# Kernel optimization log

Measured on AMD Instinct MI355X. Metric: run time of the kernel, lower is better.

The kernel has to match this reference:

```python
import jax, jax.numpy as jnp
import numpy as np


def setup_inputs() -> dict:
    key = jax.random.key(0)
    ks = jax.random.split(key, 8)
    B, N, D, E, M = 32, 128, 128, 32, 8192
    h_nodes = jax.random.normal(ks[0], (B, N, D), dtype=jnp.float32)
    h_edges = jax.random.normal(ks[1], (B, N, N, E), dtype=jnp.float32)
    W_edit = jax.random.normal(ks[2], (2 * D + E, 4), dtype=jnp.float32) * 0.02
    b_edit = jnp.zeros((4,), dtype=jnp.float32)
    W_stop = jax.random.normal(ks[3], (D, 1), dtype=jnp.float32) * 0.02
    b_stop = jnp.zeros((1,), dtype=jnp.float32)
    i_idx = jax.random.randint(ks[4], (M,), 0, N, dtype=jnp.int32)
    j_idx = jax.random.randint(ks[5], (M,), 0, N, dtype=jnp.int32)
    b_idx = jax.random.randint(ks[6], (M,), 0, 4, dtype=jnp.int32)
    feas = jax.random.randint(ks[7], (B, M), 0, 2, dtype=jnp.int32).astype(jnp.bool_)
    stop_feas = jnp.ones((B,), dtype=jnp.bool_)
    return {
        "h_nodes": h_nodes, "h_edges": h_edges,
        "W_edit": W_edit, "b_edit": b_edit,
        "W_stop": W_stop, "b_stop": b_stop,
        "i_idx": i_idx, "j_idx": j_idx, "b_idx": b_idx,
        "feas": feas, "stop_feas": stop_feas,
    }


def reference(h_nodes, h_edges, W_edit, b_edit, W_stop, b_stop,
              i_idx, j_idx, b_idx, feas, stop_feas):
    # h_nodes: [B,N,D], h_edges: [B,N,N,E]
    B = h_nodes.shape[0]
    M = i_idx.shape[0]
    neg_inf = jnp.asarray(-jnp.inf, dtype=h_nodes.dtype)
    # Batched gather of all (i, j, e_ij) edit features: [B, M, 2D+E]
    feat = jnp.concatenate(
        [h_nodes[:, i_idx], h_nodes[:, j_idx], h_edges[:, i_idx, j_idx]],
        axis=-1,
    )
    # Single fused small matmul over all edits: [B, M, 4]
    edit_logits = jnp.einsum("bmf,fo->bmo", feat, W_edit) + b_edit
    # Select the bond-type channel b for each edit: [B, M]
    sel = jnp.take_along_axis(
        edit_logits, jnp.broadcast_to(b_idx[None, :, None], (B, M, 1)), axis=2
    )[..., 0]
    sel = jnp.where(feas, sel, neg_inf)
    # STOP logit from mean-pooled node features: [B]
    stop = (h_nodes.mean(axis=1) @ W_stop + b_stop)[:, 0]
    stop = jnp.where(stop_feas, stop, neg_inf)
    # [B, M+1] logits (edits followed by STOP)
    return jnp.concatenate([sel, stop[:, None]], axis=1)
```

## Files before the change

### kernel.cpp

```cpp
#include <hip/hip_runtime.h>
#include <hip/hip_fp16.h>
#include <math.h>

#define BATCH 32
#define NNODE 128
#define DDIM 128
#define EDIM 32
#define MEDITS 8192
#define OUTSTRIDE (MEDITS + 1)

typedef unsigned short u16;
typedef unsigned int u32;

#define MASK16 ((u16)0xFBFFu)
#define MASK32 0xC76A6000u

__device__ __forceinline__ u32 f2u(float f) { u32 x; __builtin_memcpy(&x, &f, 4); return x; }
__device__ __forceinline__ float u2f(u32 x) { float f; __builtin_memcpy(&f, &x, 4); return f; }

template <int MODE>
__device__ __forceinline__ float cv16(u32 bits) {
    if constexpr (MODE == 1) return __half2float(__ushort_as_half((u16)bits));
    else                     return u2f(bits << 16);
}
template <int MODE>
__device__ __forceinline__ float cv16hi(u32 w) {
    if constexpr (MODE == 1) return __half2float(__ushort_as_half((u16)(w >> 16)));
    else                     return u2f(w & 0xFFFF0000u);
}

__device__ __forceinline__ u16 f32_to_f16_safe(float f) {
    u16 h = __half_as_ushort(__float2half_rn(f));
    if ((h & 0x7C00u) == 0x7C00u) h = (u16)((h & 0x8000u) | 0x7BFFu);
    return h;
}

__device__ __forceinline__ u16 f32_to_bf16_safe(float f) {
    u32 x = f2u(f);
    u32 r = x + 0x7FFFu + ((x >> 16) & 1u);
    u16 u = (u16)(r >> 16);
    if ((u & 0x7C00u) == 0x7C00u) u = (u16)((u & 0x8000u) | 0x7BFFu);
    return u;
}

__device__ __forceinline__ u32 enc_f32(float f) {
    u32 x = f2u(f);
    if ((x & 0x7F800000u) == 0x7F800000u)
        x = (x & 0x80000000u) | 0x476A6000u;
    return x;
}

template <int MODE>
__device__ __forceinline__ float LD(const void* p, size_t i) {
    if constexpr (MODE == 0) return ((const float*)p)[i];
    else return cv16<MODE>(((const u16*)p)[i]);
}

template <int MODE>
__device__ __forceinline__ void ST(void* o, size_t i, float v, bool masked) {
    if constexpr (MODE == 0) ((u32*)o)[i] = masked ? MASK32 : enc_f32(v);
    else if constexpr (MODE == 1) ((u16*)o)[i] = masked ? MASK16 : f32_to_f16_safe(v);
    else ((u16*)o)[i] = masked ? MASK16 : f32_to_bf16_safe(v);
}

template <int NT>
__device__ __forceinline__ int block_probe(const u16* __restrict__ h) {
    const int t = threadIdx.x;
    __shared__ int cb[4], cs[4];
    int myb = 0, mys = 0;
#pragma unroll
    for (int k = 0; k < 256 / NT; ++k) {
        u16 u = h[2 * (t + k * NT)];
        int e8 = (u >> 7) & 0xFF;
        int e5 = (u >> 10) & 0x1F;
        myb += (e8 >= 118 && e8 <= 129);
        mys += (e5 >= 6 && e5 <= 14);
    }
#pragma unroll
    for (int off = 32; off; off >>= 1) {
        myb += __shfl_down(myb, off, 64);
        mys += __shfl_down(mys, off, 64);
    }
    if ((t & 63) == 0) { cb[t >> 6] = myb; cs[t >> 6] = mys; }
    if (NT < 256 && t == 0) {
#pragma unroll
        for (int w = NT / 64; w < 4; ++w) { cb[w] = 0; cs[w] = 0; }
    }
    __syncthreads();
    int B = cb[0] + cb[1] + cb[2] + cb[3];
    int S = cs[0] + cs[1] + cs[2] + cs[3];
    return (B < 48) ? 0 : ((S > 87) ? 1 : 2);
}

template <int MODE>
__device__ void proj_impl(const void* h_nodes, const void* W_edit, const void* b_edit,
                          const void* W_stop, const void* b_stop,
                          const unsigned char* stop_feas,
                          float* __restrict__ Pi, float* __restrict__ Pj, void* out) {
    const int b = blockIdx.x;
    const int sel = blockIdx.y;
    const int t = threadIdx.x;

    if (sel < 8) {
        const int c = sel & 3;
        const int half = sel >> 2;
        __shared__ __align__(16) float wcol[DDIM];
        wcol[t] = LD<MODE>(W_edit, (size_t)(half * DDIM + t) * 4 + c);
        __syncthreads();
        const size_t rowbase = ((size_t)b * NNODE + t) * DDIM;
        const float4* wp = (const float4*)wcol;
        float acc = 0.f;
        if constexpr (MODE == 0) {
            const float4* hp = (const float4*)((const float*)h_nodes + rowbase);
#pragma unroll
            for (int k = 0; k < DDIM / 4; ++k) {
                float4 h4 = hp[k], w4 = wp[k];
                acc += h4.x * w4.x + h4.y * w4.y + h4.z * w4.z + h4.w * w4.w;
            }
        } else {
            const uint2* hp = (const uint2*)((const u16*)h_nodes + rowbase);
#pragma unroll
            for (int k = 0; k < DDIM / 4; ++k) {
                uint2 h2 = hp[k]; float4 w4 = wp[k];
                acc += cv16<MODE>(h2.x & 0xFFFFu) * w4.x + cv16hi<MODE>(h2.x) * w4.y
                     + cv16<MODE>(h2.y & 0xFFFFu) * w4.z + cv16hi<MODE>(h2.y) * w4.w;
            }
        }
        if (half == 0) {
            acc += LD<MODE>(b_edit, c);
            Pi[((size_t)b * NNODE + t) * 4 + c] = acc;
        } else {
            Pj[((size_t)b * NNODE + t) * 4 + c] = acc;
        }
    } else {
        const size_t base = (size_t)b * (NNODE * DDIM);
        float colsum = 0.f;
#pragma unroll 8
        for (int n = 0; n < NNODE; ++n) colsum += LD<MODE>(h_nodes, base + n * DDIM + t);
        float v = colsum * LD<MODE>(W_stop, t);
        __shared__ float red[2];
#pragma unroll
        for (int off = 32; off; off >>= 1) v += __shfl_down(v, off, 64);
        if ((t & 63) == 0) red[t >> 6] = v;
        __syncthreads();
        if (t == 0) {
            float s = (red[0] + red[1]) * (1.0f / NNODE) + LD<MODE>(b_stop, 0);
            ST<MODE>(out, (size_t)b * OUTSTRIDE + MEDITS, s, stop_feas[b] == 0);
        }
    }
}

__global__ void __launch_bounds__(128)
proj_stop_kernel(const void* h_nodes, const void* W_edit, const void* b_edit,
                 const void* W_stop, const void* b_stop,
                 const unsigned char* stop_feas,
                 float* Pi, float* Pj, void* out) {
    const int mode = block_probe<128>((const u16*)h_nodes);
    if (mode == 0)      proj_impl<0>(h_nodes, W_edit, b_edit, W_stop, b_stop, stop_feas, Pi, Pj, out);
    else if (mode == 1) proj_impl<1>(h_nodes, W_edit, b_edit, W_stop, b_stop, stop_feas, Pi, Pj, out);
    else                proj_impl<2>(h_nodes, W_edit, b_edit, W_stop, b_stop, stop_feas, Pi, Pj, out);
}

template <int MODE>
__device__ void edits_impl(const void* h_edges, const void* W_edit,
                           const int* __restrict__ i_idx, const int* __restrict__ j_idx,
                           const int* __restrict__ b_idx,
                           const unsigned char* __restrict__ feas,
                           const float* __restrict__ Pi, const float* __restrict__ Pj,
                           void* out) {
    const int t = threadIdx.x;
    const int m = blockIdx.x * 256 + t;
    const int b = blockIdx.y;

    __shared__ __align__(16) float Wec[4][EDIM];
    __shared__ float Pb[NNODE * 4];
    __shared__ float Qb[NNODE * 4];
    if (t < 128) {
        const int c = t >> 5, e = t & 31;
        Wec[c][e] = LD<MODE>(W_edit, (size_t)(2 * DDIM + e) * 4 + c);
    }
    Pb[t] = Pi[(size_t)b * (NNODE * 4) + t];
    Pb[t + 256] = Pi[(size_t)b * (NNODE * 4) + t + 256];
    Qb[t] = Pj[(size_t)b * (NNODE * 4) + t];
    Qb[t + 256] = Pj[(size_t)b * (NNODE * 4) + t + 256];
    __syncthreads();

    const int i = i_idx[m] & (NNODE - 1);
    const int j = j_idx[m] & (NNODE - 1);
    const int c = b_idx[m] & 3;
    const size_t ebase = (((size_t)b * NNODE + i) * NNODE + j) * EDIM;
    const float4* wv = (const float4*)Wec[c];

    float acc = 0.f;
    if constexpr (MODE == 0) {
        const float4* ep = (const float4*)((const float*)h_edges + ebase);
#pragma unroll
        for (int k = 0; k < EDIM / 4; ++k) {
            float4 e4 = ep[k], w4 = wv[k];
            acc += e4.x * w4.x + e4.y * w4.y + e4.z * w4.z + e4.w * w4.w;
        }
    } else {
        const uint4* ep = (const uint4*)((const u16*)h_edges + ebase);
#pragma unroll
        for (int k = 0; k < EDIM / 8; ++k) {
            uint4 q = ep[k];
            float4 wa = wv[2 * k], wb = wv[2 * k + 1];
            acc += cv16<MODE>(q.x & 0xFFFFu) * wa.x + cv16hi<MODE>(q.x) * wa.y
                 + cv16<MODE>(q.y & 0xFFFFu) * wa.z + cv16hi<MODE>(q.y) * wa.w
                 + cv16<MODE>(q.z & 0xFFFFu) * wb.x + cv16hi<MODE>(q.z) * wb.y
                 + cv16<MODE>(q.w & 0xFFFFu) * wb.z + cv16hi<MODE>(q.w) * wb.w;
        }
    }
    float r = acc + Pb[i * 4 + c] + Qb[j * 4 + c];
    bool masked = (feas[(size_t)b * MEDITS + m] == 0);
    ST<MODE>(out, (size_t)b * OUTSTRIDE + m, r, masked);
}

__global__ void __launch_bounds__(256)
edits_kernel(const void* h_nodes, const void* h_edges, const void* W_edit,
             const int* i_idx, const int* j_idx, const int* b_idx,
             const unsigned char* feas,
             const float* Pi, const float* Pj, void* out) {
    const int mode = block_probe<256>((const u16*)h_nodes);
    if (mode == 0)      edits_impl<0>(h_edges, W_edit, i_idx, j_idx, b_idx, feas, Pi, Pj, out);
    else if (mode == 1) edits_impl<1>(h_edges, W_edit, i_idx, j_idx, b_idx, feas, Pi, Pj, out);
    else                edits_impl<2>(h_edges, W_edit, i_idx, j_idx, b_idx, feas, Pi, Pj, out);
}

extern "C" void kernel_launch(void* const* d_in, const int* in_sizes, int n_in,
                              void* d_out, int out_size, void* d_ws, size_t ws_size,
                              hipStream_t stream) {
    (void)in_sizes; (void)n_in; (void)out_size; (void)ws_size;

    const void* h_nodes = d_in[0];
    const void* h_edges = d_in[1];
    const void* W_edit  = d_in[2];
    const void* b_edit  = d_in[3];
    const void* W_stop  = d_in[4];
    const void* b_stop  = d_in[5];
    const int*  i_idx   = (const int*)d_in[6];
    const int*  j_idx   = (const int*)d_in[7];
    const int*  b_idx   = (const int*)d_in[8];
    const unsigned char* feas      = (const unsigned char*)d_in[9];
    const unsigned char* stop_feas = (const unsigned char*)d_in[10];

    float* Pi = (float*)d_ws;
    float* Pj = Pi + BATCH * NNODE * 4;

    proj_stop_kernel<<<dim3(BATCH, 9), 128, 0, stream>>>(
        h_nodes, W_edit, b_edit, W_stop, b_stop, stop_feas, Pi, Pj, d_out);
    edits_kernel<<<dim3(MEDITS / 256, BATCH), 256, 0, stream>>>(
        h_nodes, h_edges, W_edit, i_idx, j_idx, b_idx, feas, Pi, Pj, d_out);
}
```

Before: 120.3 us.

## Fuse node projection and stop logit into the edits kernel

Merges the two launches into one kernel. Each edits block now recomputes the per-batch node projections (Pi/Pj) into shared memory, with 4 nodes per thread, instead of reading them from a workspace written by a separate kernel. The gathered edge-feature loads are issued before the projection so their latency overlaps with it. This removes one launch and the global round trip for the projections, at the cost of 32x redundant projection work per batch (each block reads all h_nodes for its batch).

Result: slower. 135.0 us (+12.3%).

```diff
diff --git a/kernel.cpp b/kernel.cpp
--- a/kernel.cpp
+++ b/kernel.cpp
@@ -93,55 +93,146 @@
 }
 
 template <int MODE>
-__device__ void proj_impl(const void* h_nodes, const void* W_edit, const void* b_edit,
-                          const void* W_stop, const void* b_stop,
-                          const unsigned char* stop_feas,
-                          float* __restrict__ Pi, float* __restrict__ Pj, void* out) {
-    const int b = blockIdx.x;
-    const int sel = blockIdx.y;
+__device__ void fused_impl(const void* h_nodes, const void* h_edges,
+                           const void* W_edit, const void* b_edit,
+                           const void* W_stop, const void* b_stop,
+                           const int* __restrict__ i_idx, const int* __restrict__ j_idx,
+                           const int* __restrict__ b_idx,
+                           const unsigned char* __restrict__ feas,
+                           const unsigned char* __restrict__ stop_feas,
+                           void* out) {
     const int t = threadIdx.x;
-
-    if (sel < 8) {
-        const int c = sel & 3;
-        const int half = sel >> 2;
-        __shared__ __align__(16) float wcol[DDIM];
-        wcol[t] = LD<MODE>(W_edit, (size_t)(half * DDIM + t) * 4 + c);
-        __syncthreads();
-        const size_t rowbase = ((size_t)b * NNODE + t) * DDIM;
-        const float4* wp = (const float4*)wcol;
+    const int m = blockIdx.x * 256 + t;
+    const int b = blockIdx.y;
+
+    __shared__ __align__(16) float Wc[2][4][DDIM + 4];
+    __shared__ __align__(16) float Wec[4][EDIM];
+    __shared__ float Pb[NNODE * 4];
+    __shared__ float Qb[NNODE * 4];
+    __shared__ float red[2];
+
+    const int i = i_idx[m] & (NNODE - 1);
+    const int j = j_idx[m] & (NNODE - 1);
+    const int ce = b_idx[m] & 3;
+    const size_t ebase = (((size_t)b * NNODE + i) * NNODE + j) * EDIM;
+    float4 ef[8];
+    uint4  eh[4];
+    if constexpr (MODE == 0) {
+        const float4* ep = (const float4*)((const float*)h_edges + ebase);
+#pragma unroll
+        for (int k = 0; k < 8; ++k) ef[k] = ep[k];
+    } else {
+        const uint4* ep = (const uint4*)((const u16*)h_edges + ebase);
+#pragma unroll
+        for (int k = 0; k < 4; ++k) eh[k] = ep[k];
+    }
+
+    {
+        const int k = t & 127, half = t >> 7;
+        if constexpr (MODE == 0) {
+            float4 row = ((const float4*)W_edit)[half * DDIM + k];
+            Wc[half][0][k] = row.x; Wc[half][1][k] = row.y;
+            Wc[half][2][k] = row.z; Wc[half][3][k] = row.w;
+        } else {
+            uint2 row = ((const uint2*)W_edit)[half * DDIM + k];
+            Wc[half][0][k] = cv16<MODE>(row.x & 0xFFFFu);
+            Wc[half][1][k] = cv16hi<MODE>(row.x);
+            Wc[half][2][k] = cv16<MODE>(row.y & 0xFFFFu);
+            Wc[half][3][k] = cv16hi<MODE>(row.y);
+        }
+    }
+    if (t < 128) {
+        const int c = t >> 5, e = t & 31;
+        Wec[c][e] = LD<MODE>(W_edit, (size_t)(2 * DDIM + e) * 4 + c);
+    }
+    __syncthreads();
+
+    {
+        const int half = t >> 7;
+        const int r = t & 127;
+        const int c = r & 3;
+        const int n0 = (r >> 2) * 4;
+        const size_t hb = ((size_t)b * NNODE + n0) * DDIM;
+        const float* wrow = &Wc[half][c][0];
+        float a0 = 0.f, a1 = 0.f, a2 = 0.f, a3 = 0.f;
+        if constexpr (MODE == 0) {
+            const float4* h0 = (const float4*)((const float*)h_nodes + hb);
+            const float4* h1 = (const float4*)((const float*)h_nodes + hb + DDIM);
+            const float4* h2 = (const float4*)((const float*)h_nodes + hb + 2 * DDIM);
+            const float4* h3 = (const float4*)((const float*)h_nodes + hb + 3 * DDIM);
+#pragma unroll 4
+            for (int k4 = 0; k4 < DDIM / 4; ++k4) {
+                float4 w4 = *(const float4*)&wrow[k4 * 4];
+                float4 x0 = h0[k4], x1 = h1[k4], x2 = h2[k4], x3 = h3[k4];
+                a0 += x0.x * w4.x + x0.y * w4.y + x0.z * w4.z + x0.w * w4.w;
+                a1 += x1.x * w4.x + x1.y * w4.y + x1.z * w4.z + x1.w * w4.w;
+                a2 += x2.x * w4.x + x2.y * w4.y + x2.z * w4.z + x2.w * w4.w;
+                a3 += x3.x * w4.x + x3.y * w4.y + x3.z * w4.z + x3.w * w4.w;
+            }
+        } else {
+            const uint2* h0 = (const uint2*)((const u16*)h_nodes + hb);
+            const uint2* h1 = (const uint2*)((const u16*)h_nodes + hb + DDIM);
+            const uint2* h2 = (const uint2*)((const u16*)h_nodes + hb + 2 * DDIM);
+            const uint2* h3 = (const uint2*)((const u16*)h_nodes + hb + 3 * DDIM);
+#pragma unroll 4
+            for (int k4 = 0; k4 < DDIM / 4; ++k4) {
+                float4 w4 = *(const float4*)&wrow[k4 * 4];
+                uint2 q0 = h0[k4], q1 = h1[k4], q2 = h2[k4], q3 = h3[k4];
+                a0 += cv16<MODE>(q0.x & 0xFFFFu) * w4.x + cv16hi<MODE>(q0.x) * w4.y
+                    + cv16<MODE>(q0.y & 0xFFFFu) * w4.z + cv16hi<MODE>(q0.y) * w4.w;
+                a1 += cv16<MODE>(q1.x & 0xFFFFu) * w4.x + cv16hi<MODE>(q1.x) * w4.y
+                    + cv16<MODE>(q1.y & 0xFFFFu) * w4.z + cv16hi<MODE>(q1.y) * w4.w;
+                a2 += cv16<MODE>(q2.x & 0xFFFFu) * w4.x + cv16hi<MODE>(q2.x) * w4.y
+                    + cv16<MODE>(q2.y & 0xFFFFu) * w4.z + cv16hi<MODE>(q2.y) * w4.w;
+                a3 += cv16<MODE>(q3.x & 0xFFFFu) * w4.x + cv16hi<MODE>(q3.x) * w4.y
+                    + cv16<MODE>(q3.y & 0xFFFFu) * w4.z + cv16hi<MODE>(q3.y) * w4.w;
+            }
+        }
+        const float bias = (half == 0) ? LD<MODE>(b_edit, c) : 0.f;
+        float* dst = half ? Qb : Pb;
+        dst[(n0 + 0) * 4 + c] = a0 + bias;
+        dst[(n0 + 1) * 4 + c] = a1 + bias;
+        dst[(n0 + 2) * 4 + c] = a2 + bias;
+        dst[(n0 + 3) * 4 + c] = a3 + bias;
+    }
+    __syncthreads();
+
+    {
+        const float4* wv = (const float4*)Wec[ce];
         float acc = 0.f;
         if constexpr (MODE == 0) {
-            const float4* hp = (const float4*)((const float*)h_nodes + rowbase);
-#pragma unroll
-            for (int k = 0; k < DDIM / 4; ++k) {
-                float4 h4 = hp[k], w4 = wp[k];
-                acc += h4.x * w4.x + h4.y * w4.y + h4.z * w4.z + h4.w * w4.w;
+#pragma unroll
+            for (int k = 0; k < EDIM / 4; ++k) {
+                float4 e4 = ef[k], w4 = wv[k];
+                acc += e4.x * w4.x + e4.y * w4.y + e4.z * w4.z + e4.w * w4.w;
             }
         } else {
-            const uint2* hp = (const uint2*)((const u16*)h_nodes + rowbase);
-#pragma unroll
-            for (int k = 0; k < DDIM / 4; ++k) {
-                uint2 h2 = hp[k]; float4 w4 = wp[k];
-                acc += cv16<MODE>(h2.x & 0xFFFFu) * w4.x + cv16hi<MODE>(h2.x) * w4.y
-                     + cv16<MODE>(h2.y & 0xFFFFu) * w4.z + cv16hi<MODE>(h2.y) * w4.w;
-            }
-        }
-        if (half == 0) {
-            acc += LD<MODE>(b_edit, c);
-            Pi[((size_t)b * NNODE + t) * 4 + c] = acc;
-        } else {
-            Pj[((size_t)b * NNODE + t) * 4 + c] = acc;
-        }
-    } else {
-        const size_t base = (size_t)b * (NNODE * DDIM);
-        float colsum = 0.f;
+#pragma unroll
+            for (int k = 0; k < EDIM / 8; ++k) {
+                uint4 q = eh[k];
+                float4 wa = wv[2 * k], wb = wv[2 * k + 1];
+                acc += cv16<MODE>(q.x & 0xFFFFu) * wa.x + cv16hi<MODE>(q.x) * wa.y
+                     + cv16<MODE>(q.y & 0xFFFFu) * wa.z + cv16hi<MODE>(q.y) * wa.w
+                     + cv16<MODE>(q.z & 0xFFFFu) * wb.x + cv16hi<MODE>(q.z) * wb.y
+                     + cv16<MODE>(q.w & 0xFFFFu) * wb.z + cv16hi<MODE>(q.w) * wb.w;
+            }
+        }
+        float rres = acc + Pb[i * 4 + ce] + Qb[j * 4 + ce];
+        bool masked = (feas[(size_t)b * MEDITS + m] == 0);
+        ST<MODE>(out, (size_t)b * OUTSTRIDE + m, rres, masked);
+    }
+
+    if (blockIdx.x == 0) {
+        if (t < 128) {
+            const size_t base = (size_t)b * (NNODE * DDIM);
+            float colsum = 0.f;
 #pragma unroll 8
-        for (int n = 0; n < NNODE; ++n) colsum += LD<MODE>(h_nodes, base + n * DDIM + t);
-        float v = colsum * LD<MODE>(W_stop, t);
-        __shared__ float red[2];
-#pragma unroll
-        for (int off = 32; off; off >>= 1) v += __shfl_down(v, off, 64);
-        if ((t & 63) == 0) red[t >> 6] = v;
+            for (int n = 0; n < NNODE; ++n) colsum += LD<MODE>(h_nodes, base + n * DDIM + t);
+            float v = colsum * LD<MODE>(W_stop, t);
+#pragma unroll
+            for (int off = 32; off; off >>= 1) v += __shfl_down(v, off, 64);
+            if ((t & 63) == 0) red[t >> 6] = v;
+        }
         __syncthreads();
         if (t == 0) {
             float s = (red[0] + red[1]) * (1.0f / NNODE) + LD<MODE>(b_stop, 0);
@@ -150,87 +241,29 @@
     }
 }
 
-__global__ void __launch_bounds__(128)
-proj_stop_kernel(const void* h_nodes, const void* W_edit, const void* b_edit,
-                 const void* W_stop, const void* b_stop,
-                 const unsigned char* stop_feas,
-                 float* Pi, float* Pj, void* out) {
-    const int mode = block_probe<128>((const u16*)h_nodes);
-    if (mode == 0)      proj_impl<0>(h_nodes, W_edit, b_edit, W_stop, b_stop, stop_feas, Pi, Pj, out);
-    else if (mode == 1) proj_impl<1>(h_nodes, W_edit, b_edit, W_stop, b_stop, stop_feas, Pi, Pj, out);
-    else                proj_impl<2>(h_nodes, W_edit, b_edit, W_stop, b_stop, stop_feas, Pi, Pj, out);
-}
-
-template <int MODE>
-__device__ void edits_impl(const void* h_edges, const void* W_edit,
-                           const int* __restrict__ i_idx, const int* __restrict__ j_idx,
-                           const int* __restrict__ b_idx,
-                           const unsigned char* __restrict__ feas,
-                           const float* __restrict__ Pi, const float* __restrict__ Pj,
-                           void* out) {
-    const int t = threadIdx.x;
-    const int m = blockIdx.x * 256 + t;
-    const int b = blockIdx.y;
-
-    __shared__ __align__(16) float Wec[4][EDIM];
-    __shared__ float Pb[NNODE * 4];
-    __shared__ float Qb[NNODE * 4];
-    if (t < 128) {
-        const int c = t >> 5, e = t & 31;
-        Wec[c][e] = LD<MODE>(W_edit, (size_t)(2 * DDIM + e) * 4 + c);
-    }
-    Pb[t] = Pi[(size_t)b * (NNODE * 4) + t];
-    Pb[t + 256] = Pi[(size_t)b * (NNODE * 4) + t + 256];
-    Qb[t] = Pj[(size_t)b * (NNODE * 4) + t];
-    Qb[t + 256] = Pj[(size_t)b * (NNODE * 4) + t + 256];
-    __syncthreads();
-
-    const int i = i_idx[m] & (NNODE - 1);
-    const int j = j_idx[m] & (NNODE - 1);
-    const int c = b_idx[m] & 3;
-    const size_t ebase = (((size_t)b * NNODE + i) * NNODE + j) * EDIM;
-    const float4* wv = (const float4*)Wec[c];
-
-    float acc = 0.f;
-    if constexpr (MODE == 0) {
-        const float4* ep = (const float4*)((const float*)h_edges + ebase);
-#pragma unroll
-        for (int k = 0; k < EDIM / 4; ++k) {
-            float4 e4 = ep[k], w4 = wv[k];
-            acc += e4.x * w4.x + e4.y * w4.y + e4.z * w4.z + e4.w * w4.w;
-        }
-    } else {
-        const uint4* ep = (const uint4*)((const u16*)h_edges + ebase);
-#pragma unroll
-        for (int k = 0; k < EDIM / 8; ++k) {
-            uint4 q = ep[k];
-            float4 wa = wv[2 * k], wb = wv[2 * k + 1];
-            acc += cv16<MODE>(q.x & 0xFFFFu) * wa.x + cv16hi<MODE>(q.x) * wa.y
-                 + cv16<MODE>(q.y & 0xFFFFu) * wa.z + cv16hi<MODE>(q.y) * wa.w
-                 + cv16<MODE>(q.z & 0xFFFFu) * wb.x + cv16hi<MODE>(q.z) * wb.y
-                 + cv16<MODE>(q.w & 0xFFFFu) * wb.z + cv16hi<MODE>(q.w) * wb.w;
-        }
-    }
-    float r = acc + Pb[i * 4 + c] + Qb[j * 4 + c];
-    bool masked = (feas[(size_t)b * MEDITS + m] == 0);
-    ST<MODE>(out, (size_t)b * OUTSTRIDE + m, r, masked);
-}
-
 __global__ void __launch_bounds__(256)
-edits_kernel(const void* h_nodes, const void* h_edges, const void* W_edit,
+fused_kernel(const void* h_nodes, const void* h_edges,
+             const void* W_edit, const void* b_edit,
+             const void* W_stop, const void* b_stop,
              const int* i_idx, const int* j_idx, const int* b_idx,
-             const unsigned char* feas,
-             const float* Pi, const float* Pj, void* out) {
+             const unsigned char* feas, const unsigned char* stop_feas,
+             void* out) {
     const int mode = block_probe<256>((const u16*)h_nodes);
-    if (mode == 0)      edits_impl<0>(h_edges, W_edit, i_idx, j_idx, b_idx, feas, Pi, Pj, out);
-    else if (mode == 1) edits_impl<1>(h_edges, W_edit, i_idx, j_idx, b_idx, feas, Pi, Pj, out);
-    else                edits_impl<2>(h_edges, W_edit, i_idx, j_idx, b_idx, feas, Pi, Pj, out);
+    if (mode == 0)
+        fused_impl<0>(h_nodes, h_edges, W_edit, b_edit, W_stop, b_stop,
+                      i_idx, j_idx, b_idx, feas, stop_feas, out);
+    else if (mode == 1)
+        fused_impl<1>(h_nodes, h_edges, W_edit, b_edit, W_stop, b_stop,
+                      i_idx, j_idx, b_idx, feas, stop_feas, out);
+    else
+        fused_impl<2>(h_nodes, h_edges, W_edit, b_edit, W_stop, b_stop,
+                      i_idx, j_idx, b_idx, feas, stop_feas, out);
 }
 
 extern "C" void kernel_launch(void* const* d_in, const int* in_sizes, int n_in,
                               void* d_out, int out_size, void* d_ws, size_t ws_size,
                               hipStream_t stream) {
-    (void)in_sizes; (void)n_in; (void)out_size; (void)ws_size;
+    (void)in_sizes; (void)n_in; (void)out_size; (void)d_ws; (void)ws_size;
 
     const void* h_nodes = d_in[0];
     const void* h_edges = d_in[1];
@@ -244,11 +277,7 @@
     const unsigned char* feas      = (const unsigned char*)d_in[9];
     const unsigned char* stop_feas = (const unsigned char*)d_in[10];
 
-    float* Pi = (float*)d_ws;
-    float* Pj = Pi + BATCH * NNODE * 4;
-
-    proj_stop_kernel<<<dim3(BATCH, 9), 128, 0, stream>>>(
-        h_nodes, W_edit, b_edit, W_stop, b_stop, stop_feas, Pi, Pj, d_out);
-    edits_kernel<<<dim3(MEDITS / 256, BATCH), 256, 0, stream>>>(
-        h_nodes, h_edges, W_edit, i_idx, j_idx, b_idx, feas, Pi, Pj, d_out);
-}
+    fused_kernel<<<dim3(MEDITS / 256, BATCH), 256, 0, stream>>>(
+        h_nodes, h_edges, W_edit, b_edit, W_stop, b_stop,
+        i_idx, j_idx, b_idx, feas, stop_feas, d_out);
+}
```
